# Optimization experiments

Measured on AMD Instinct MI355X. Metric: run time of the kernel, lower is better.

## Reference

```python
import jax, jax.numpy as jnp
import numpy as np

B, N, HID, H, FFN, E = 1, 50000, 96, 8, 384, 800000
D = HID // H
SCALE = float(np.sqrt(D))


def _layernorm(x, g, b, eps=1e-5):
    mu = jnp.mean(x, axis=-1, keepdims=True)
    var = jnp.var(x, axis=-1, keepdims=True)
    return (x - mu) * jax.lax.rsqrt(var + eps) * g + b


def setup_inputs() -> dict:
    key = jax.random.key(0)
    ks = jax.random.split(key, 20)
    std = 0.02
    inp = {
        "x": jax.random.normal(ks[0], (B, N, HID), dtype=jnp.float32),
        "edge_index": jax.random.randint(ks[1], (2, E), 0, B * N, dtype=jnp.int32),
        "ln1_g": jnp.ones((HID,), jnp.float32),
        "ln1_b": jnp.zeros((HID,), jnp.float32),
        "Wq": jax.random.normal(ks[2], (HID, HID), jnp.float32) * std,
        "bq": jnp.zeros((HID,), jnp.float32),
        "Wk": jax.random.normal(ks[3], (HID, HID), jnp.float32) * std,
        "bk": jnp.zeros((HID,), jnp.float32),
        "Wv": jax.random.normal(ks[4], (HID, HID), jnp.float32) * std,
        "bv": jnp.zeros((HID,), jnp.float32),
        "Wo": jax.random.normal(ks[5], (HID, HID), jnp.float32) * std,
        "bo": jnp.zeros((HID,), jnp.float32),
        "ln2_g": jnp.ones((HID,), jnp.float32),
        "ln2_b": jnp.zeros((HID,), jnp.float32),
        "W1": jax.random.normal(ks[6], (HID, FFN), jnp.float32) * std,
        "b1": jnp.zeros((FFN,), jnp.float32),
        "W2": jax.random.normal(ks[7], (FFN, HID), jnp.float32) * std,
        "b2": jnp.zeros((HID,), jnp.float32),
    }
    return inp


def _sparse_attn(q, k, v, edge_index):
    # q,k,v: [B*N, H, D]; edge_index: [2, E]
    src_idx = edge_index[0].astype(jnp.int32)
    dst_idx = edge_index[1].astype(jnp.int32)
    src = k[src_idx]                                # [E, H, D]
    dest = q[dst_idx]                               # [E, H, D]
    score = jnp.sum(src * dest, axis=-1, keepdims=True) / SCALE  # [E, H, 1]
    score = jnp.exp(jnp.clip(score, -5.0, 5.0))
    msg = v[src_idx] * score                        # [E, H, D]
    wV = jax.ops.segment_sum(msg, dst_idx, num_segments=B * N)   # [B*N, H, D]
    Z = jax.ops.segment_sum(score, dst_idx, num_segments=B * N)  # [B*N, H, 1]
    return wV / (Z + 1e-6)


def reference(x, edge_index, ln1_g, ln1_b, Wq, bq, Wk, bk, Wv, bv, Wo, bo,
              ln2_g, ln2_b, W1, b1, W2, b2):
    # --- self-attention block ---
    y = _layernorm(x, ln1_g, ln1_b)                 # [B, N, HID]
    q = (y @ Wq + bq).reshape(B * N, H, D)
    k = (y @ Wk + bk).reshape(B * N, H, D)
    v = (y @ Wv + bv).reshape(B * N, H, D)
    a = _sparse_attn(q, k, v, edge_index)           # [B*N, H, D]
    a = a.reshape(B, N, HID)
    y = a @ Wo + bo
    x = x + y
    # --- FFN block ---
    y = _layernorm(x, ln2_g, ln2_b)
    y = jax.nn.gelu(y @ W1 + b1, approximate=False)
    y = y @ W2 + b2
    return x + y
```

## Files before the change

### kernel.cpp

```cpp
#include <hip/hip_runtime.h>
#include <hip/hip_bf16.h>
#include <math.h>

#define NN 50000
#define HIDD 96
#define NH 8
#define HD 12
#define FFND 384
#define NE 800000
#define NB 98
#define BSTRIDE 12288

#define INV_SCALE 0.28867513459481287f
#define LOG2E 1.4426950408889634f

typedef short short8 __attribute__((ext_vector_type(8)));
typedef float f32x4 __attribute__((ext_vector_type(4)));
typedef float f32x2 __attribute__((ext_vector_type(2)));

__device__ __forceinline__ float bf2f(unsigned short u) {
    union { unsigned int i; float f; } c;
    c.i = ((unsigned int)u) << 16;
    return c.f;
}

__global__ __launch_bounds__(256) void prep(
    int* __restrict__ gcursor,
    const float* __restrict__ Wq, const float* __restrict__ Wk,
    const float* __restrict__ Wv, const float* __restrict__ Wo,
    const float* __restrict__ W1, const float* __restrict__ W2,
    __hip_bfloat16* __restrict__ wbuf,
    const float* __restrict__ x, const float* __restrict__ g1,
    const float* __restrict__ b1, __hip_bfloat16* __restrict__ ybf) {
    int b = blockIdx.x;
    int t = threadIdx.x;
    if (b == 0) {
        if (t < 128) gcursor[t] = t * BSTRIDE;
        return;
    }
    if (b < 433) {
        int idx = b - 1;
        const float* W; __hip_bfloat16* D; int K, N; int i;
        if (idx < 144)      { W = W1; D = wbuf + 36864; K = 96;  N = 384; i = idx * 256 + t; }
        else if (idx < 288) { W = W2; D = wbuf + 73728; K = 384; N = 96;  i = (idx - 144) * 256 + t; }
        else {
            int slab = (idx - 288) / 36;
            W = (slab == 0) ? Wq : (slab == 1) ? Wk : (slab == 2) ? Wv : Wo;
            D = wbuf + slab * 9216; K = 96; N = 96;
            i = ((idx - 288) % 36) * 256 + t;
        }
        if (i < K * N) {
            int n = i / K, k = i % K;
            D[i] = __float2bfloat16(W[k * N + n]);
        }
    } else {
        int row = (b - 433) * 4 + (t >> 6);
        int lane = t & 63;
        if (row >= NN) return;
        const float* xr = x + (size_t)row * HIDD;
        float v0 = xr[lane];
        float v1 = (lane < 32) ? xr[64 + lane] : 0.0f;
        float s = v0 + v1, q = v0 * v0 + v1 * v1;
#pragma unroll
        for (int o = 32; o > 0; o >>= 1) {
            s += __shfl_xor(s, o);
            q += __shfl_xor(q, o);
        }
        float mean = s * (1.0f / 96.0f);
        float var = q * (1.0f / 96.0f) - mean * mean;
        float rs = rsqrtf(var + 1e-5f);
        __hip_bfloat16* yr = ybf + (size_t)row * HIDD;
        yr[lane] = __float2bfloat16((v0 - mean) * rs * g1[lane] + b1[lane]);
        if (lane < 32)
            yr[64 + lane] = __float2bfloat16((v1 - mean) * rs * g1[64 + lane] + b1[64 + lane]);
    }
}

template<int K, int EPI, int SMODE>
__device__ __forceinline__ void gemm_body(
    const __hip_bfloat16* __restrict__ A, const __hip_bfloat16* __restrict__ BT,
    const float* __restrict__ bias, const __hip_bfloat16* __restrict__ R,
    void* __restrict__ Cptr, int ldc, int col0, int koff, int xb) {
    constexpr int BK = (K > 192) ? 192 : K;
    __shared__ __hip_bfloat16 Bs[96][BK + 8];
    int t = threadIdx.x;
    int lane = t & 63, wave = t >> 6;
    int row0 = xb * 128 + wave * 32;
    int lr = lane & 15, kg = lane >> 4;
    bool val0 = (row0 + 16 <= NN);
    bool val1 = (row0 + 32 <= NN);
    int ra0 = val0 ? row0 : 0;
    int ra1 = val1 ? (row0 + 16) : 0;
    const __hip_bfloat16* A0 = A + (size_t)(ra0 + lr) * K + kg * 8;
    const __hip_bfloat16* A1 = A + (size_t)(ra1 + lr) * K + kg * 8;
    f32x4 acc[2][6];
#pragma unroll
    for (int f = 0; f < 2; f++)
#pragma unroll
        for (int ct = 0; ct < 6; ct++) acc[f][ct] = (f32x4){0.f, 0.f, 0.f, 0.f};

    for (int k0 = 0; k0 < K; k0 += BK) {
        for (int i = t * 8; i < 96 * BK; i += 256 * 8) {
            int r = i / BK, c = i % BK;
            *(short8*)&Bs[r][c] = *(const short8*)&BT[(size_t)r * K + k0 + c];
        }
        __syncthreads();
#pragma unroll
        for (int kc = 0; kc < BK; kc += 32) {
            short8 a0 = *(const short8*)(A0 + k0 + kc);
            short8 a1 = *(const short8*)(A1 + k0 + kc);
#pragma unroll
            for (int ct = 0; ct < 6; ct++) {
                short8 bf_ = *(const short8*)&Bs[ct * 16 + lr][kc + kg * 8];
                acc[0][ct] = __builtin_amdgcn_mfma_f32_16x16x32_bf16(a0, bf_, acc[0][ct], 0, 0, 0);
                acc[1][ct] = __builtin_amdgcn_mfma_f32_16x16x32_bf16(a1, bf_, acc[1][ct], 0, 0, 0);
            }
        }
        __syncthreads();
    }

#pragma unroll
    for (int f = 0; f < 2; f++) {
        if (f == 0 ? !val0 : !val1) continue;
        int crow = row0 + f * 16 + kg * 4;
#pragma unroll
        for (int ct = 0; ct < 6; ct++) {
            int col = col0 + ct * 16 + lr;
            float bb = bias[col];
#pragma unroll
            for (int r = 0; r < 4; r++) {
                float o = acc[f][ct][r] + bb;
                if (EPI == 1)
                    o = 0.5f * o * (1.0f + erff(o * 0.70710678118654752f));
                if (EPI == 2)
                    o += __bfloat162float(R[(size_t)(crow + r) * 96 + col]);
                if (SMODE == 0)
                    ((float*)Cptr)[(size_t)(crow + r) * ldc + col] = o;
                else if (SMODE == 1)
                    ((__hip_bfloat16*)Cptr)[(size_t)(crow + r) * ldc + col] = __float2bfloat16(o);
                else {
                    unsigned int enc = (unsigned int)__builtin_amdgcn_cvt_pk_fp8_f32(o, o, 0, false);
                    ((unsigned char*)Cptr)[(size_t)(crow + r) * 192 + ((col - col0) / 12) * 24 + koff + ((col - col0) % 12)]
                        = (unsigned char)(enc & 0xffu);
                }
            }
        }
    }
}

__global__ __launch_bounds__(256) void scatter_qkv(
    const int* __restrict__ ei, int* __restrict__ gcursor,
    unsigned int* __restrict__ ebuf,
    const __hip_bfloat16* __restrict__ A, const __hip_bfloat16* __restrict__ wbuf,
    const float* __restrict__ bq, const float* __restrict__ bk,
    const float* __restrict__ bv,
    __hip_bfloat16* __restrict__ qbf, unsigned char* __restrict__ kv) {
    int b = blockIdx.x;
    if (b < 391) {
        __shared__ int lcount[128];
        __shared__ int lbase[128];
        int t = threadIdx.x;
        int e0 = b * 2048;
        if (t < 128) lcount[t] = 0;
        __syncthreads();
        int rank[8], dsts[8], srcv[8];
#pragma unroll
        for (int i = 0; i < 8; i++) {
            int e = e0 + t + i * 256;
            if (e < NE) {
                srcv[i] = ei[e];
                int d = ei[NE + e];
                dsts[i] = d;
                rank[i] = atomicAdd(&lcount[d >> 9], 1);
            } else dsts[i] = -1;
        }
        __syncthreads();
        if (t < 128) lbase[t] = lcount[t] ? atomicAdd(&gcursor[t], lcount[t]) : 0;
        __syncthreads();
#pragma unroll
        for (int i = 0; i < 8; i++) {
            if (dsts[i] >= 0) {
                int bk_ = dsts[i] >> 9;
                ebuf[lbase[bk_] + rank[i]] =
                    ((unsigned int)dsts[i] << 16) | (unsigned int)srcv[i];
            }
        }
    } else {
        int idx = b - 391;
        int y = idx / 391, xb = idx % 391;
        if (y == 0)
            gemm_body<96, 0, 1>(A, wbuf, bq, nullptr, qbf, 96, 0, 0, xb);
        else if (y == 1)
            gemm_body<96, 0, 2>(A, wbuf + 9216, bk, nullptr, kv, 0, 0, 0, xb);
        else
            gemm_body<96, 0, 2>(A, wbuf + 18432, bv, nullptr, kv, 0, 0, 12, xb);
    }
}

__global__ __launch_bounds__(1024) void bucket_build(
    const unsigned int* __restrict__ ebuf, const int* __restrict__ gcursor,
    uint2* __restrict__ rowrange, unsigned short* __restrict__ srcs) {
    __shared__ int cnt[512];
    int b = blockIdx.x;
    int t = threadIdx.x;
    int n0 = b * 512;
    int beg = b * BSTRIDE;
    int end = gcursor[b];
    if (t < 512) cnt[t] = 0;
    __syncthreads();
    for (int e = beg + t; e < end; e += 1024)
        atomicAdd(&cnt[(ebuf[e] >> 16) - n0], 1);
    __syncthreads();
    int my = (t < 512) ? cnt[t] : 0;
    for (int off = 1; off < 512; off <<= 1) {
        int v = (t >= off && t < 512) ? cnt[t - off] : 0;
        __syncthreads();
        if (t < 512) cnt[t] += v;
        __syncthreads();
    }
    int excl = (t > 0 && t < 512) ? cnt[t - 1] : 0;
    int base = beg + excl;
    if (t < 512 && n0 + t < NN)
        rowrange[n0 + t] = make_uint2((unsigned)base, (unsigned)(base + my));
    __syncthreads();
    if (t < 512) cnt[t] = base;
    __syncthreads();
    for (int e = beg + t; e < end; e += 1024) {
        unsigned int u = ebuf[e];
        int pos = atomicAdd(&cnt[(u >> 16) - n0], 1);
        srcs[pos] = (unsigned short)(u & 0xffffu);
    }
}

__global__ __launch_bounds__(256) void proj_ln(
    const __hip_bfloat16* __restrict__ A, const __hip_bfloat16* __restrict__ BT,
    const float* __restrict__ bias, const float* __restrict__ R,
    const float* __restrict__ g2, const float* __restrict__ b2v,
    __hip_bfloat16* __restrict__ x2, __hip_bfloat16* __restrict__ ybf) {
    constexpr int K = 96;
    __shared__ __hip_bfloat16 Bs[96][K + 8];
    int t = threadIdx.x;
    int lane = t & 63, wave = t >> 6;
    int row0 = blockIdx.x * 128 + wave * 32;
    int lr = lane & 15, kg = lane >> 4;
    bool val0 = (row0 + 16 <= NN);
    bool val1 = (row0 + 32 <= NN);
    int ra0 = val0 ? row0 : 0;
    int ra1 = val1 ? (row0 + 16) : 0;
    const __hip_bfloat16* A0 = A + (size_t)(ra0 + lr) * K + kg * 8;
    const __hip_bfloat16* A1 = A + (size_t)(ra1 + lr) * K + kg * 8;
    f32x4 acc[2][6];
#pragma unroll
    for (int f = 0; f < 2; f++)
#pragma unroll
        for (int ct = 0; ct < 6; ct++) acc[f][ct] = (f32x4){0.f, 0.f, 0.f, 0.f};

    for (int i = t * 8; i < 96 * K; i += 256 * 8) {
        int r = i / K, c = i % K;
        *(short8*)&Bs[r][c] = *(const short8*)&BT[(size_t)r * K + c];
    }
    __syncthreads();
#pragma unroll
    for (int kc = 0; kc < K; kc += 32) {
        short8 a0 = *(const short8*)(A0 + kc);
        short8 a1 = *(const short8*)(A1 + kc);
#pragma unroll
        for (int ct = 0; ct < 6; ct++) {
            short8 bf_ = *(const short8*)&Bs[ct * 16 + lr][kc + kg * 8];
            acc[0][ct] = __builtin_amdgcn_mfma_f32_16x16x32_bf16(a0, bf_, acc[0][ct], 0, 0, 0);
            acc[1][ct] = __builtin_amdgcn_mfma_f32_16x16x32_bf16(a1, bf_, acc[1][ct], 0, 0, 0);
        }
    }

    float bo_[6], gv[6], bv_[6];
#pragma unroll
    for (int ct = 0; ct < 6; ct++) {
        int col = ct * 16 + lr;
        bo_[ct] = bias[col];
        gv[ct]  = g2[col];
        bv_[ct] = b2v[col];
    }
#pragma unroll
    for (int f = 0; f < 2; f++) {
        if (f == 0 ? !val0 : !val1) continue;
        int crow = row0 + f * 16 + kg * 4;
#pragma unroll
        for (int r = 0; r < 4; r++) {
            int row = crow + r;
            float o[6], s1 = 0.f, s2 = 0.f;
#pragma unroll
            for (int ct = 0; ct < 6; ct++) {
                int col = ct * 16 + lr;
                float val = acc[f][ct][r] + bo_[ct] + R[(size_t)row * 96 + col];
                o[ct] = val; s1 += val; s2 += val * val;
            }
#pragma unroll
            for (int m = 1; m < 16; m <<= 1) {
                s1 += __shfl_xor(s1, m);
                s2 += __shfl_xor(s2, m);
            }
            float mu = s1 * (1.0f / 96.0f);
            float var = s2 * (1.0f / 96.0f) - mu * mu;
            float rs = rsqrtf(var + 1e-5f);
#pragma unroll
            for (int ct = 0; ct < 6; ct++) {
                int col = ct * 16 + lr;
                x2[(size_t)row * 96 + col] = __float2bfloat16(o[ct]);
                ybf[(size_t)row * 96 + col] =
                    __float2bfloat16((o[ct] - mu) * rs * gv[ct] + bv_[ct]);
            }
        }
    }
}

__global__ __launch_bounds__(256) void ffn_fused(
    const __hip_bfloat16* __restrict__ ybf, const __hip_bfloat16* __restrict__ W1T,
    const __hip_bfloat16* __restrict__ W2T, const float* __restrict__ b1,
    const float* __restrict__ b2v, const __hip_bfloat16* __restrict__ x2,
    float* __restrict__ out) {
    __shared__ __hip_bfloat16 hlds[64][392];
    __shared__ __hip_bfloat16 Bs[96][104];
    int t = threadIdx.x, lane = t & 63, wave = t >> 6;
    int row0 = blockIdx.x * 64;
    int lr = lane & 15, kg = lane >> 4;
    int rw = row0 + wave * 16;
    bool valid = (rw + 16 <= NN);
    int ra = valid ? rw : 0;

    short8 af[3];
#pragma unroll
    for (int kc = 0; kc < 3; kc++)
        af[kc] = *(const short8*)&ybf[(size_t)(ra + lr) * 96 + kc * 32 + kg * 8];

    for (int s = 0; s < 4; s++) {
        for (int i = t * 8; i < 96 * 96; i += 256 * 8) {
            int r = i / 96, c = i % 96;
            *(short8*)&Bs[r][c] = *(const short8*)&W1T[(size_t)(s * 96 + r) * 96 + c];
        }
        __syncthreads();
        f32x4 acc[6];
#pragma unroll
        for (int ct = 0; ct < 6; ct++) acc[ct] = (f32x4){0.f, 0.f, 0.f, 0.f};
#pragma unroll
        for (int kc = 0; kc < 3; kc++) {
#pragma unroll
            for (int ct = 0; ct < 6; ct++) {
                short8 bf_ = *(const short8*)&Bs[ct * 16 + lr][kc * 32 + kg * 8];
                acc[ct] = __builtin_amdgcn_mfma_f32_16x16x32_bf16(af[kc], bf_, acc[ct], 0, 0, 0);
            }
        }
#pragma unroll
        for (int ct = 0; ct < 6; ct++) {
            int col = s * 96 + ct * 16 + lr;
            float bb = b1[col];
#pragma unroll
            for (int r = 0; r < 4; r++) {
                float o = acc[ct][r] + bb;
                o = 0.5f * o * (1.0f + erff(o * 0.70710678118654752f));
                hlds[wave * 16 + kg * 4 + r][col] = __float2bfloat16(o);
            }
        }
        __syncthreads();
    }

    f32x4 acc2[6];
#pragma unroll
    for (int ct = 0; ct < 6; ct++) acc2[ct] = (f32x4){0.f, 0.f, 0.f, 0.f};
    for (int c = 0; c < 4; c++) {
        for (int i = t * 8; i < 96 * 96; i += 256 * 8) {
            int r = i / 96, cc = i % 96;
            *(short8*)&Bs[r][cc] = *(const short8*)&W2T[(size_t)r * 384 + c * 96 + cc];
        }
        __syncthreads();
#pragma unroll
        for (int kc = 0; kc < 3; kc++) {
            short8 a = *(const short8*)&hlds[wave * 16 + lr][c * 96 + kc * 32 + kg * 8];
#pragma unroll
            for (int ct = 0; ct < 6; ct++) {
                short8 bf_ = *(const short8*)&Bs[ct * 16 + lr][kc * 32 + kg * 8];
                acc2[ct] = __builtin_amdgcn_mfma_f32_16x16x32_bf16(a, bf_, acc2[ct], 0, 0, 0);
            }
        }
        __syncthreads();
    }

    if (valid) {
        int crow = rw + kg * 4;
#pragma unroll
        for (int ct = 0; ct < 6; ct++) {
            int col = ct * 16 + lr;
            float bb = b2v[col];
#pragma unroll
            for (int r = 0; r < 4; r++) {
                float o = acc2[ct][r] + bb
                        + __bfloat162float(x2[(size_t)(crow + r) * 96 + col]);
                out[(size_t)(crow + r) * 96 + col] = o;
            }
        }
    }
}

__global__ __launch_bounds__(256) void attn_gather(
    const __hip_bfloat16* __restrict__ qbf, const unsigned char* __restrict__ kv,
    const uint2* __restrict__ rowrange, const unsigned short* __restrict__ srcs,
    __hip_bfloat16* __restrict__ abf) {
    int wave = (blockIdx.x * blockDim.x + threadIdx.x) >> 6;
    int lane = threadIdx.x & 63;
    if (wave >= NN) return;
    int dst = wave;
    int h = lane & 7;
    int eslot = lane >> 3;
    float qf[12];
    {
        const uint2* qp = (const uint2*)(qbf + (size_t)dst * HIDD + h * HD);
        uint2 u0 = qp[0], u1 = qp[1], u2 = qp[2];
        unsigned int w[6] = {u0.x, u0.y, u1.x, u1.y, u2.x, u2.y};
#pragma unroll
        for (int i = 0; i < 6; i++) {
            qf[2 * i]     = bf2f((unsigned short)(w[i] & 0xffffu));
            qf[2 * i + 1] = bf2f((unsigned short)(w[i] >> 16));
        }
    }
    uint2 rr = rowrange[dst];
    int beg = (int)rr.x, end = (int)rr.y;
    float acc[12];
#pragma unroll
    for (int i = 0; i < 12; i++) acc[i] = 0.0f;
    float zz = 0.0f;

    int e = beg + eslot;
    bool has = e < end;
    uint2 cA, cB, cC;
    if (has) {
        int src = (int)srcs[e];
        const uint2* kp = (const uint2*)(kv + (size_t)src * 192 + h * 24);
        cA = kp[0]; cB = kp[1]; cC = kp[2];
    }
    while (has) {
        int en = e + 8;
        bool hasn = en < end;
        uint2 nA, nB, nC;
        if (hasn) {
            int srcn = (int)srcs[en];
            const uint2* kp = (const uint2*)(kv + (size_t)srcn * 192 + h * 24);
            nA = kp[0]; nB = kp[1]; nC = kp[2];
        }
        f32x2 p;
        float dot = 0.0f;
        p = __builtin_amdgcn_cvt_pk_f32_fp8(cA.x, false); dot += p[0] * qf[0]  + p[1] * qf[1];
        p = __builtin_amdgcn_cvt_pk_f32_fp8(cA.x, true);  dot += p[0] * qf[2]  + p[1] * qf[3];
        p = __builtin_amdgcn_cvt_pk_f32_fp8(cA.y, false); dot += p[0] * qf[4]  + p[1] * qf[5];
        p = __builtin_amdgcn_cvt_pk_f32_fp8(cA.y, true);  dot += p[0] * qf[6]  + p[1] * qf[7];
        p = __builtin_amdgcn_cvt_pk_f32_fp8(cB.x, false); dot += p[0] * qf[8]  + p[1] * qf[9];
        p = __builtin_amdgcn_cvt_pk_f32_fp8(cB.x, true);  dot += p[0] * qf[10] + p[1] * qf[11];
        float s = fminf(fmaxf(dot * INV_SCALE, -5.0f), 5.0f);
        float sc = exp2f(s * LOG2E);
        p = __builtin_amdgcn_cvt_pk_f32_fp8(cB.y, false); acc[0]  += p[0] * sc; acc[1]  += p[1] * sc;
        p = __builtin_amdgcn_cvt_pk_f32_fp8(cB.y, true);  acc[2]  += p[0] * sc; acc[3]  += p[1] * sc;
        p = __builtin_amdgcn_cvt_pk_f32_fp8(cC.x, false); acc[4]  += p[0] * sc; acc[5]  += p[1] * sc;
        p = __builtin_amdgcn_cvt_pk_f32_fp8(cC.x, true);  acc[6]  += p[0] * sc; acc[7]  += p[1] * sc;
        p = __builtin_amdgcn_cvt_pk_f32_fp8(cC.y, false); acc[8]  += p[0] * sc; acc[9]  += p[1] * sc;
        p = __builtin_amdgcn_cvt_pk_f32_fp8(cC.y, true);  acc[10] += p[0] * sc; acc[11] += p[1] * sc;
        zz += sc;
        cA = nA; cB = nB; cC = nC;
        e = en; has = hasn;
    }
#pragma unroll
    for (int m = 8; m < 64; m <<= 1) {
#pragma unroll
        for (int i = 0; i < 12; i++) acc[i] += __shfl_xor(acc[i], m);
        zz += __shfl_xor(zz, m);
    }
    if (eslot == 0) {
        float inv = 1.0f / (zz + 1e-6f);
        __hip_bfloat16* ar = abf + (size_t)dst * HIDD + h * HD;
#pragma unroll
        for (int i = 0; i < 12; i++) ar[i] = __float2bfloat16(acc[i] * inv);
    }
}

extern "C" void kernel_launch(void* const* d_in, const int* in_sizes, int n_in,
                              void* d_out, int out_size, void* d_ws, size_t ws_size,
                              hipStream_t stream) {
    const float* x     = (const float*)d_in[0];
    const int*   ei    = (const int*)d_in[1];
    const float* ln1_g = (const float*)d_in[2];
    const float* ln1_b = (const float*)d_in[3];
    const float* Wq    = (const float*)d_in[4];
    const float* bq    = (const float*)d_in[5];
    const float* Wk    = (const float*)d_in[6];
    const float* bk    = (const float*)d_in[7];
    const float* Wv    = (const float*)d_in[8];
    const float* bv    = (const float*)d_in[9];
    const float* Wo    = (const float*)d_in[10];
    const float* bo    = (const float*)d_in[11];
    const float* ln2_g = (const float*)d_in[12];
    const float* ln2_b = (const float*)d_in[13];
    const float* W1    = (const float*)d_in[14];
    const float* b1    = (const float*)d_in[15];
    const float* W2    = (const float*)d_in[16];
    const float* b2    = (const float*)d_in[17];
    float* out = (float*)d_out;

    float* ws = (float*)d_ws;
    const size_t NF = (size_t)NN * HIDD;
    __hip_bfloat16* qbf = (__hip_bfloat16*)ws;
    unsigned char*  kv  = (unsigned char*)(ws + NF / 2);
    __hip_bfloat16* abf = (__hip_bfloat16*)(ws + NF / 2 + NF);
    __hip_bfloat16* x2  = (__hip_bfloat16*)(ws + 2 * NF);
    __hip_bfloat16* ybf = (__hip_bfloat16*)(ws + 2 * NF + NF / 2);
    int* ibase = (int*)(ws + 3 * NF);
    uint2* rowrange = (uint2*)ibase;
    unsigned short* srcs = (unsigned short*)(ibase + 2 * NN);
    int* gcursor = ibase + 2 * NN + (NB * BSTRIDE + 1) / 2;
    unsigned int* ebuf = (unsigned int*)(gcursor + 128);
    __hip_bfloat16* wbuf = (__hip_bfloat16*)(ws + 3 * NF + NF / 2);
    __hip_bfloat16* WoT = wbuf + 27648;
    __hip_bfloat16* W1T = wbuf + 36864;
    __hip_bfloat16* W2T = wbuf + 73728;

    const int MT = (NN + 127) / 128;
    const int FT = (NN + 63) / 64;

    prep<<<433 + 12500, 256, 0, stream>>>(gcursor, Wq, Wk, Wv, Wo, W1, W2, wbuf,
                                          x, ln1_g, ln1_b, ybf);
    scatter_qkv<<<391 + 3 * MT, 256, 0, stream>>>(ei, gcursor, ebuf,
                                                  ybf, wbuf, bq, bk, bv, qbf, kv);
    bucket_build<<<NB, 1024, 0, stream>>>(ebuf, gcursor, rowrange, srcs);
    attn_gather<<<(NN + 3) / 4, 256, 0, stream>>>(qbf, kv, rowrange, srcs, abf);
    proj_ln<<<MT, 256, 0, stream>>>(abf, WoT, bo, x, ln2_g, ln2_b, x2, ybf);
    ffn_fused<<<FT, 256, 0, stream>>>(ybf, W1T, W2T, b1, b2, x2, out);
}
```

Baseline: 143.1 us.

## Split fused FFN into two persistent kernels with LDS-resident weight slabs

Replaces the single fused FFN kernel with two persistent kernels. ffn1_p keeps one 96-column slab of W1 in LDS per block and writes GELU output to a global bf16 hidden buffer. ffn2_p keeps a 48-column slab of W2 in LDS, reads the hidden buffer back and adds the residual. The goal is to stop reloading the weights per 64-row tile, cut the barriers, and give each wave two 16-row fragments for more MFMA reuse. The cost is a round trip of about 38 MB of hidden activations through global memory, stored in workspace that reuses the dead q/kv/attention buffers.

```diff
diff --git a/kernel.cpp b/kernel.cpp
--- a/kernel.cpp
+++ b/kernel.cpp
@@ -313,88 +313,122 @@
     }
 }
 
-__global__ __launch_bounds__(256) void ffn_fused(
+__global__ __launch_bounds__(256) void ffn1_p(
     const __hip_bfloat16* __restrict__ ybf, const __hip_bfloat16* __restrict__ W1T,
-    const __hip_bfloat16* __restrict__ W2T, const float* __restrict__ b1,
+    const float* __restrict__ b1, __hip_bfloat16* __restrict__ hbf) {
+    __shared__ __hip_bfloat16 Bs[96][104];
+    int t = threadIdx.x, lane = t & 63, wave = t >> 6;
+    int s = blockIdx.y;
+    int lr = lane & 15, kg = lane >> 4;
+    const __hip_bfloat16* slab = W1T + (size_t)s * 96 * 96;
+    for (int i = t * 8; i < 96 * 96; i += 256 * 8) {
+        int r = i / 96, c = i % 96;
+        *(short8*)&Bs[r][c] = *(const short8*)&slab[r * 96 + c];
+    }
+    __syncthreads();
+    float bb[6];
+#pragma unroll
+    for (int ct = 0; ct < 6; ct++) bb[ct] = b1[s * 96 + ct * 16 + lr];
+
+    for (int tile = blockIdx.x; tile < 391; tile += 98) {
+        int row0 = tile * 128 + wave * 32;
+        bool val0 = (row0 + 16 <= NN);
+        bool val1 = (row0 + 32 <= NN);
+        int ra0 = val0 ? row0 : 0;
+        int ra1 = val1 ? (row0 + 16) : 0;
+        short8 a0[3], a1[3];
+#pragma unroll
+        for (int kc = 0; kc < 3; kc++) {
+            a0[kc] = *(const short8*)&ybf[(size_t)(ra0 + lr) * 96 + kc * 32 + kg * 8];
+            a1[kc] = *(const short8*)&ybf[(size_t)(ra1 + lr) * 96 + kc * 32 + kg * 8];
+        }
+        f32x4 acc[2][6];
+#pragma unroll
+        for (int f = 0; f < 2; f++)
+#pragma unroll
+            for (int ct = 0; ct < 6; ct++) acc[f][ct] = (f32x4){0.f, 0.f, 0.f, 0.f};
+#pragma unroll
+        for (int kc = 0; kc < 3; kc++) {
+#pragma unroll
+            for (int ct = 0; ct < 6; ct++) {
+                short8 bf_ = *(const short8*)&Bs[ct * 16 + lr][kc * 32 + kg * 8];
+                acc[0][ct] = __builtin_amdgcn_mfma_f32_16x16x32_bf16(a0[kc], bf_, acc[0][ct], 0, 0, 0);
+                acc[1][ct] = __builtin_amdgcn_mfma_f32_16x16x32_bf16(a1[kc], bf_, acc[1][ct], 0, 0, 0);
+            }
+        }
+#pragma unroll
+        for (int f = 0; f < 2; f++) {
+            if (f == 0 ? !val0 : !val1) continue;
+            int crow = row0 + f * 16 + kg * 4;
+#pragma unroll
+            for (int ct = 0; ct < 6; ct++) {
+                int col = s * 96 + ct * 16 + lr;
+#pragma unroll
+                for (int r = 0; r < 4; r++) {
+                    float o = acc[f][ct][r] + bb[ct];
+                    o = 0.5f * o * (1.0f + erff(o * 0.70710678118654752f));
+                    hbf[(size_t)(crow + r) * FFND + col] = __float2bfloat16(o);
+                }
+            }
+        }
+    }
+}
+
+__global__ __launch_bounds__(256) void ffn2_p(
+    const __hip_bfloat16* __restrict__ hbf, const __hip_bfloat16* __restrict__ W2T,
     const float* __restrict__ b2v, const __hip_bfloat16* __restrict__ x2,
     float* __restrict__ out) {
-    __shared__ __hip_bfloat16 hlds[64][392];
-    __shared__ __hip_bfloat16 Bs[96][104];
+    __shared__ __hip_bfloat16 Bs[4][48][104];
     int t = threadIdx.x, lane = t & 63, wave = t >> 6;
-    int row0 = blockIdx.x * 64;
+    int ch = blockIdx.y;
     int lr = lane & 15, kg = lane >> 4;
-    int rw = row0 + wave * 16;
-    bool valid = (rw + 16 <= NN);
-    int ra = valid ? rw : 0;
-
-    short8 af[3];
-#pragma unroll
-    for (int kc = 0; kc < 3; kc++)
-        af[kc] = *(const short8*)&ybf[(size_t)(ra + lr) * 96 + kc * 32 + kg * 8];
-
-    for (int s = 0; s < 4; s++) {
-        for (int i = t * 8; i < 96 * 96; i += 256 * 8) {
-            int r = i / 96, c = i % 96;
-            *(short8*)&Bs[r][c] = *(const short8*)&W1T[(size_t)(s * 96 + r) * 96 + c];
-        }
-        __syncthreads();
-        f32x4 acc[6];
-#pragma unroll
-        for (int ct = 0; ct < 6; ct++) acc[ct] = (f32x4){0.f, 0.f, 0.f, 0.f};
-#pragma unroll
-        for (int kc = 0; kc < 3; kc++) {
-#pragma unroll
-            for (int ct = 0; ct < 6; ct++) {
-                short8 bf_ = *(const short8*)&Bs[ct * 16 + lr][kc * 32 + kg * 8];
-                acc[ct] = __builtin_amdgcn_mfma_f32_16x16x32_bf16(af[kc], bf_, acc[ct], 0, 0, 0);
-            }
-        }
-#pragma unroll
-        for (int ct = 0; ct < 6; ct++) {
-            int col = s * 96 + ct * 16 + lr;
-            float bb = b1[col];
-#pragma unroll
-            for (int r = 0; r < 4; r++) {
-                float o = acc[ct][r] + bb;
-                o = 0.5f * o * (1.0f + erff(o * 0.70710678118654752f));
-                hlds[wave * 16 + kg * 4 + r][col] = __float2bfloat16(o);
-            }
-        }
-        __syncthreads();
-    }
-
-    f32x4 acc2[6];
-#pragma unroll
-    for (int ct = 0; ct < 6; ct++) acc2[ct] = (f32x4){0.f, 0.f, 0.f, 0.f};
-    for (int c = 0; c < 4; c++) {
-        for (int i = t * 8; i < 96 * 96; i += 256 * 8) {
-            int r = i / 96, cc = i % 96;
-            *(short8*)&Bs[r][cc] = *(const short8*)&W2T[(size_t)r * 384 + c * 96 + cc];
-        }
-        __syncthreads();
-#pragma unroll
-        for (int kc = 0; kc < 3; kc++) {
-            short8 a = *(const short8*)&hlds[wave * 16 + lr][c * 96 + kc * 32 + kg * 8];
-#pragma unroll
-            for (int ct = 0; ct < 6; ct++) {
-                short8 bf_ = *(const short8*)&Bs[ct * 16 + lr][kc * 32 + kg * 8];
-                acc2[ct] = __builtin_amdgcn_mfma_f32_16x16x32_bf16(a, bf_, acc2[ct], 0, 0, 0);
-            }
-        }
-        __syncthreads();
-    }
-
-    if (valid) {
-        int crow = rw + kg * 4;
-#pragma unroll
-        for (int ct = 0; ct < 6; ct++) {
-            int col = ct * 16 + lr;
-            float bb = b2v[col];
-#pragma unroll
-            for (int r = 0; r < 4; r++) {
-                float o = acc2[ct][r] + bb
-                        + __bfloat162float(x2[(size_t)(crow + r) * 96 + col]);
-                out[(size_t)(crow + r) * 96 + col] = o;
+    const __hip_bfloat16* wslab = W2T + (size_t)ch * 48 * 384;
+    for (int i = t * 8; i < 48 * 384; i += 256 * 8) {
+        int r = i / 384, c = i % 384;
+        *(short8*)&Bs[c / 96][r][c % 96] = *(const short8*)&wslab[(size_t)r * 384 + c];
+    }
+    __syncthreads();
+    float bb[3];
+#pragma unroll
+    for (int ct = 0; ct < 3; ct++) bb[ct] = b2v[ch * 48 + ct * 16 + lr];
+
+    for (int tile = blockIdx.x; tile < 391; tile += 196) {
+        int row0 = tile * 128 + wave * 32;
+        bool val0 = (row0 + 16 <= NN);
+        bool val1 = (row0 + 32 <= NN);
+        int ra0 = val0 ? row0 : 0;
+        int ra1 = val1 ? (row0 + 16) : 0;
+        const __hip_bfloat16* H0 = hbf + (size_t)(ra0 + lr) * FFND + kg * 8;
+        const __hip_bfloat16* H1 = hbf + (size_t)(ra1 + lr) * FFND + kg * 8;
+        f32x4 acc[2][3];
+#pragma unroll
+        for (int f = 0; f < 2; f++)
+#pragma unroll
+            for (int ct = 0; ct < 3; ct++) acc[f][ct] = (f32x4){0.f, 0.f, 0.f, 0.f};
+#pragma unroll
+        for (int kc = 0; kc < 12; kc++) {
+            short8 a0 = *(const short8*)(H0 + kc * 32);
+            short8 a1 = *(const short8*)(H1 + kc * 32);
+#pragma unroll
+            for (int ct = 0; ct < 3; ct++) {
+                short8 bf_ = *(const short8*)&Bs[kc / 3][ct * 16 + lr][(kc % 3) * 32 + kg * 8];
+                acc[0][ct] = __builtin_amdgcn_mfma_f32_16x16x32_bf16(a0, bf_, acc[0][ct], 0, 0, 0);
+                acc[1][ct] = __builtin_amdgcn_mfma_f32_16x16x32_bf16(a1, bf_, acc[1][ct], 0, 0, 0);
+            }
+        }
+#pragma unroll
+        for (int f = 0; f < 2; f++) {
+            if (f == 0 ? !val0 : !val1) continue;
+            int crow = row0 + f * 16 + kg * 4;
+#pragma unroll
+            for (int ct = 0; ct < 3; ct++) {
+                int col = ch * 48 + ct * 16 + lr;
+#pragma unroll
+                for (int r = 0; r < 4; r++) {
+                    float o = acc[f][ct][r] + bb[ct]
+                            + __bfloat162float(x2[(size_t)(crow + r) * 96 + col]);
+                    out[(size_t)(crow + r) * 96 + col] = o;
+                }
             }
         }
     }
@@ -507,6 +541,7 @@
     __hip_bfloat16* qbf = (__hip_bfloat16*)ws;
     unsigned char*  kv  = (unsigned char*)(ws + NF / 2);
     __hip_bfloat16* abf = (__hip_bfloat16*)(ws + NF / 2 + NF);
+    __hip_bfloat16* hbf = (__hip_bfloat16*)ws;
     __hip_bfloat16* x2  = (__hip_bfloat16*)(ws + 2 * NF);
     __hip_bfloat16* ybf = (__hip_bfloat16*)(ws + 2 * NF + NF / 2);
     int* ibase = (int*)(ws + 3 * NF);
@@ -520,7 +555,6 @@
     __hip_bfloat16* W2T = wbuf + 73728;
 
     const int MT = (NN + 127) / 128;
-    const int FT = (NN + 63) / 64;
 
     prep<<<433 + 12500, 256, 0, stream>>>(gcursor, Wq, Wk, Wv, Wo, W1, W2, wbuf,
                                           x, ln1_g, ln1_b, ybf);
@@ -529,5 +563,12 @@
     bucket_build<<<NB, 1024, 0, stream>>>(ebuf, gcursor, rowrange, srcs);
     attn_gather<<<(NN + 3) / 4, 256, 0, stream>>>(qbf, kv, rowrange, srcs, abf);
     proj_ln<<<MT, 256, 0, stream>>>(abf, WoT, bo, x, ln2_g, ln2_b, x2, ybf);
-    ffn_fused<<<FT, 256, 0, stream>>>(ybf, W1T, W2T, b1, b2, x2, out);
-}
+    {
+        dim3 g(98, 4);
+        ffn1_p<<<g, 256, 0, stream>>>(ybf, W1T, b1, hbf);
+    }
+    {
+        dim3 g(196, 2);
+        ffn2_p<<<g, 256, 0, stream>>>(hbf, W2T, b2, x2, out);
+    }
+}
```

New measurement: 139.3 us. 1.03x faster.

## Merge QKV GEMM blocks and split fused FFN into two kernels

Applied to the files above, without the earlier changes.

The QKV projection now runs one block per 128-row tile that loads A fragments once and loops over the three weight slabs, replacing three separate blocks that each reloaded A. The fused FFN kernel, which kept the 384-wide hidden activations in a large LDS buffer, is split into ffn1_p, which writes the GELU output to a bf16 global buffer reusing workspace, and ffn2_p, which reads it back and does the second GEMM in two column chunks. The split is meant to cut LDS use and raise occupancy. In exchange it adds a roughly 38 MB global round trip and one more kernel launch.

```diff
diff --git a/kernel.cpp b/kernel.cpp
--- a/kernel.cpp
+++ b/kernel.cpp
@@ -76,78 +76,6 @@
     }
 }
 
-template<int K, int EPI, int SMODE>
-__device__ __forceinline__ void gemm_body(
-    const __hip_bfloat16* __restrict__ A, const __hip_bfloat16* __restrict__ BT,
-    const float* __restrict__ bias, const __hip_bfloat16* __restrict__ R,
-    void* __restrict__ Cptr, int ldc, int col0, int koff, int xb) {
-    constexpr int BK = (K > 192) ? 192 : K;
-    __shared__ __hip_bfloat16 Bs[96][BK + 8];
-    int t = threadIdx.x;
-    int lane = t & 63, wave = t >> 6;
-    int row0 = xb * 128 + wave * 32;
-    int lr = lane & 15, kg = lane >> 4;
-    bool val0 = (row0 + 16 <= NN);
-    bool val1 = (row0 + 32 <= NN);
-    int ra0 = val0 ? row0 : 0;
-    int ra1 = val1 ? (row0 + 16) : 0;
-    const __hip_bfloat16* A0 = A + (size_t)(ra0 + lr) * K + kg * 8;
-    const __hip_bfloat16* A1 = A + (size_t)(ra1 + lr) * K + kg * 8;
-    f32x4 acc[2][6];
-#pragma unroll
-    for (int f = 0; f < 2; f++)
-#pragma unroll
-        for (int ct = 0; ct < 6; ct++) acc[f][ct] = (f32x4){0.f, 0.f, 0.f, 0.f};
-
-    for (int k0 = 0; k0 < K; k0 += BK) {
-        for (int i = t * 8; i < 96 * BK; i += 256 * 8) {
-            int r = i / BK, c = i % BK;
-            *(short8*)&Bs[r][c] = *(const short8*)&BT[(size_t)r * K + k0 + c];
-        }
-        __syncthreads();
-#pragma unroll
-        for (int kc = 0; kc < BK; kc += 32) {
-            short8 a0 = *(const short8*)(A0 + k0 + kc);
-            short8 a1 = *(const short8*)(A1 + k0 + kc);
-#pragma unroll
-            for (int ct = 0; ct < 6; ct++) {
-                short8 bf_ = *(const short8*)&Bs[ct * 16 + lr][kc + kg * 8];
-                acc[0][ct] = __builtin_amdgcn_mfma_f32_16x16x32_bf16(a0, bf_, acc[0][ct], 0, 0, 0);
-                acc[1][ct] = __builtin_amdgcn_mfma_f32_16x16x32_bf16(a1, bf_, acc[1][ct], 0, 0, 0);
-            }
-        }
-        __syncthreads();
-    }
-
-#pragma unroll
-    for (int f = 0; f < 2; f++) {
-        if (f == 0 ? !val0 : !val1) continue;
-        int crow = row0 + f * 16 + kg * 4;
-#pragma unroll
-        for (int ct = 0; ct < 6; ct++) {
-            int col = col0 + ct * 16 + lr;
-            float bb = bias[col];
-#pragma unroll
-            for (int r = 0; r < 4; r++) {
-                float o = acc[f][ct][r] + bb;
-                if (EPI == 1)
-                    o = 0.5f * o * (1.0f + erff(o * 0.70710678118654752f));
-                if (EPI == 2)
-                    o += __bfloat162float(R[(size_t)(crow + r) * 96 + col]);
-                if (SMODE == 0)
-                    ((float*)Cptr)[(size_t)(crow + r) * ldc + col] = o;
-                else if (SMODE == 1)
-                    ((__hip_bfloat16*)Cptr)[(size_t)(crow + r) * ldc + col] = __float2bfloat16(o);
-                else {
-                    unsigned int enc = (unsigned int)__builtin_amdgcn_cvt_pk_fp8_f32(o, o, 0, false);
-                    ((unsigned char*)Cptr)[(size_t)(crow + r) * 192 + ((col - col0) / 12) * 24 + koff + ((col - col0) % 12)]
-                        = (unsigned char)(enc & 0xffu);
-                }
-            }
-        }
-    }
-}
-
 __global__ __launch_bounds__(256) void scatter_qkv(
     const int* __restrict__ ei, int* __restrict__ gcursor,
     unsigned int* __restrict__ ebuf,
@@ -156,10 +84,10 @@
     const float* __restrict__ bv,
     __hip_bfloat16* __restrict__ qbf, unsigned char* __restrict__ kv) {
     int b = blockIdx.x;
+    int t = threadIdx.x;
     if (b < 391) {
         __shared__ int lcount[128];
         __shared__ int lbase[128];
-        int t = threadIdx.x;
         int e0 = b * 2048;
         if (t < 128) lcount[t] = 0;
         __syncthreads();
@@ -186,14 +114,68 @@
             }
         }
     } else {
-        int idx = b - 391;
-        int y = idx / 391, xb = idx % 391;
-        if (y == 0)
-            gemm_body<96, 0, 1>(A, wbuf, bq, nullptr, qbf, 96, 0, 0, xb);
-        else if (y == 1)
-            gemm_body<96, 0, 2>(A, wbuf + 9216, bk, nullptr, kv, 0, 0, 0, xb);
-        else
-            gemm_body<96, 0, 2>(A, wbuf + 18432, bv, nullptr, kv, 0, 0, 12, xb);
+        __shared__ __hip_bfloat16 Bs[96][104];
+        int xb = b - 391;
+        int lane = t & 63, wave = t >> 6;
+        int row0 = xb * 128 + wave * 32;
+        int lr = lane & 15, kg = lane >> 4;
+        bool val0 = (row0 + 16 <= NN);
+        bool val1 = (row0 + 32 <= NN);
+        int ra0 = val0 ? row0 : 0;
+        int ra1 = val1 ? (row0 + 16) : 0;
+        short8 a0[3], a1[3];
+#pragma unroll
+        for (int kc = 0; kc < 3; kc++) {
+            a0[kc] = *(const short8*)&A[(size_t)(ra0 + lr) * 96 + kc * 32 + kg * 8];
+            a1[kc] = *(const short8*)&A[(size_t)(ra1 + lr) * 96 + kc * 32 + kg * 8];
+        }
+        for (int y = 0; y < 3; y++) {
+            const __hip_bfloat16* slab = wbuf + y * 9216;
+            for (int i = t * 8; i < 96 * 96; i += 256 * 8) {
+                int r = i / 96, c = i % 96;
+                *(short8*)&Bs[r][c] = *(const short8*)&slab[r * 96 + c];
+            }
+            __syncthreads();
+            f32x4 acc[2][6];
+#pragma unroll
+            for (int f = 0; f < 2; f++)
+#pragma unroll
+                for (int ct = 0; ct < 6; ct++) acc[f][ct] = (f32x4){0.f, 0.f, 0.f, 0.f};
+#pragma unroll
+            for (int kc = 0; kc < 3; kc++) {
+#pragma unroll
+                for (int ct = 0; ct < 6; ct++) {
+                    short8 bf_ = *(const short8*)&Bs[ct * 16 + lr][kc * 32 + kg * 8];
+                    acc[0][ct] = __builtin_amdgcn_mfma_f32_16x16x32_bf16(a0[kc], bf_, acc[0][ct], 0, 0, 0);
+                    acc[1][ct] = __builtin_amdgcn_mfma_f32_16x16x32_bf16(a1[kc], bf_, acc[1][ct], 0, 0, 0);
+                }
+            }
+            const float* bias = (y == 0) ? bq : (y == 1) ? bk : bv;
+            int koff = (y == 2) ? 12 : 0;
+#pragma unroll
+            for (int f = 0; f < 2; f++) {
+                if (f == 0 ? !val0 : !val1) continue;
+                int crow = row0 + f * 16 + kg * 4;
+#pragma unroll
+                for (int ct = 0; ct < 6; ct++) {
+                    int col = ct * 16 + lr;
+                    float bb = bias[col];
+#pragma unroll
+                    for (int r = 0; r < 4; r++) {
+                        float o = acc[f][ct][r] + bb;
+                        if (y == 0) {
+                            qbf[(size_t)(crow + r) * HIDD + col] = __float2bfloat16(o);
+                        } else {
+                            unsigned int enc =
+                                (unsigned int)__builtin_amdgcn_cvt_pk_fp8_f32(o, o, 0, false);
+                            kv[(size_t)(crow + r) * 192 + (col / 12) * 24 + koff + (col % 12)]
+                                = (unsigned char)(enc & 0xffu);
+                        }
+                    }
+                }
+            }
+            __syncthreads();
+        }
     }
 }
 
@@ -313,29 +295,25 @@
     }
 }
 
-__global__ __launch_bounds__(256) void ffn_fused(
+__global__ __launch_bounds__(256) void ffn1_p(
     const __hip_bfloat16* __restrict__ ybf, const __hip_bfloat16* __restrict__ W1T,
-    const __hip_bfloat16* __restrict__ W2T, const float* __restrict__ b1,
-    const float* __restrict__ b2v, const __hip_bfloat16* __restrict__ x2,
-    float* __restrict__ out) {
-    __shared__ __hip_bfloat16 hlds[64][392];
+    const float* __restrict__ b1, __hip_bfloat16* __restrict__ hbf) {
     __shared__ __hip_bfloat16 Bs[96][104];
     int t = threadIdx.x, lane = t & 63, wave = t >> 6;
-    int row0 = blockIdx.x * 64;
     int lr = lane & 15, kg = lane >> 4;
-    int rw = row0 + wave * 16;
-    bool valid = (rw + 16 <= NN);
-    int ra = valid ? rw : 0;
-
+    int row0 = blockIdx.x * 64 + wave * 16;
+    bool valid = (row0 + 16 <= NN);
+    int ra = valid ? row0 : 0;
     short8 af[3];
 #pragma unroll
     for (int kc = 0; kc < 3; kc++)
         af[kc] = *(const short8*)&ybf[(size_t)(ra + lr) * 96 + kc * 32 + kg * 8];
 
     for (int s = 0; s < 4; s++) {
+        const __hip_bfloat16* slab = W1T + (size_t)s * 96 * 96;
         for (int i = t * 8; i < 96 * 96; i += 256 * 8) {
             int r = i / 96, c = i % 96;
-            *(short8*)&Bs[r][c] = *(const short8*)&W1T[(size_t)(s * 96 + r) * 96 + c];
+            *(short8*)&Bs[r][c] = *(const short8*)&slab[r * 96 + c];
         }
         __syncthreads();
         f32x4 acc[6];
@@ -349,54 +327,72 @@
                 acc[ct] = __builtin_amdgcn_mfma_f32_16x16x32_bf16(af[kc], bf_, acc[ct], 0, 0, 0);
             }
         }
-#pragma unroll
-        for (int ct = 0; ct < 6; ct++) {
-            int col = s * 96 + ct * 16 + lr;
-            float bb = b1[col];
-#pragma unroll
-            for (int r = 0; r < 4; r++) {
-                float o = acc[ct][r] + bb;
-                o = 0.5f * o * (1.0f + erff(o * 0.70710678118654752f));
-                hlds[wave * 16 + kg * 4 + r][col] = __float2bfloat16(o);
-            }
-        }
-        __syncthreads();
-    }
-
-    f32x4 acc2[6];
-#pragma unroll
-    for (int ct = 0; ct < 6; ct++) acc2[ct] = (f32x4){0.f, 0.f, 0.f, 0.f};
-    for (int c = 0; c < 4; c++) {
-        for (int i = t * 8; i < 96 * 96; i += 256 * 8) {
-            int r = i / 96, cc = i % 96;
-            *(short8*)&Bs[r][cc] = *(const short8*)&W2T[(size_t)r * 384 + c * 96 + cc];
-        }
-        __syncthreads();
-#pragma unroll
-        for (int kc = 0; kc < 3; kc++) {
-            short8 a = *(const short8*)&hlds[wave * 16 + lr][c * 96 + kc * 32 + kg * 8];
+        if (valid) {
+            int crow = row0 + kg * 4;
 #pragma unroll
             for (int ct = 0; ct < 6; ct++) {
-                short8 bf_ = *(const short8*)&Bs[ct * 16 + lr][kc * 32 + kg * 8];
-                acc2[ct] = __builtin_amdgcn_mfma_f32_16x16x32_bf16(a, bf_, acc2[ct], 0, 0, 0);
-            }
-        }
-        __syncthreads();
-    }
-
-    if (valid) {
-        int crow = rw + kg * 4;
-#pragma unroll
-        for (int ct = 0; ct < 6; ct++) {
-            int col = ct * 16 + lr;
-            float bb = b2v[col];
-#pragma unroll
-            for (int r = 0; r < 4; r++) {
-                float o = acc2[ct][r] + bb
-                        + __bfloat162float(x2[(size_t)(crow + r) * 96 + col]);
-                out[(size_t)(crow + r) * 96 + col] = o;
-            }
-        }
+                int col = s * 96 + ct * 16 + lr;
+                float bb = b1[col];
+#pragma unroll
+                for (int r = 0; r < 4; r++) {
+                    float o = acc[ct][r] + bb;
+                    o = 0.5f * o * (1.0f + erff(o * 0.70710678118654752f));
+                    hbf[(size_t)(crow + r) * FFND + col] = __float2bfloat16(o);
+                }
+            }
+        }
+        __syncthreads();
+    }
+}
+
+__global__ __launch_bounds__(256) void ffn2_p(
+    const __hip_bfloat16* __restrict__ hbf, const __hip_bfloat16* __restrict__ W2T,
+    const float* __restrict__ b2v, const __hip_bfloat16* __restrict__ x2,
+    float* __restrict__ out) {
+    __shared__ __hip_bfloat16 Bs[4][48][104];
+    int t = threadIdx.x, lane = t & 63, wave = t >> 6;
+    int lr = lane & 15, kg = lane >> 4;
+    int row0 = blockIdx.x * 64 + wave * 16;
+    bool valid = (row0 + 16 <= NN);
+    int ra = valid ? row0 : 0;
+    short8 hf[12];
+#pragma unroll
+    for (int kc = 0; kc < 12; kc++)
+        hf[kc] = *(const short8*)&hbf[(size_t)(ra + lr) * FFND + kc * 32 + kg * 8];
+
+    for (int ch = 0; ch < 2; ch++) {
+        const __hip_bfloat16* wslab = W2T + (size_t)ch * 48 * 384;
+        for (int i = t * 8; i < 48 * 384; i += 256 * 8) {
+            int r = i / 384, c = i % 384;
+            *(short8*)&Bs[c / 96][r][c % 96] = *(const short8*)&wslab[(size_t)r * 384 + c];
+        }
+        __syncthreads();
+        f32x4 acc[3];
+#pragma unroll
+        for (int ct = 0; ct < 3; ct++) acc[ct] = (f32x4){0.f, 0.f, 0.f, 0.f};
+#pragma unroll
+        for (int kc = 0; kc < 12; kc++) {
+#pragma unroll
+            for (int ct = 0; ct < 3; ct++) {
+                short8 bf_ = *(const short8*)&Bs[kc / 3][ct * 16 + lr][(kc % 3) * 32 + kg * 8];
+                acc[ct] = __builtin_amdgcn_mfma_f32_16x16x32_bf16(hf[kc], bf_, acc[ct], 0, 0, 0);
+            }
+        }
+        if (valid) {
+            int crow = row0 + kg * 4;
+#pragma unroll
+            for (int ct = 0; ct < 3; ct++) {
+                int col = ch * 48 + ct * 16 + lr;
+                float bb = b2v[col];
+#pragma unroll
+                for (int r = 0; r < 4; r++) {
+                    float o = acc[ct][r] + bb
+                            + __bfloat162float(x2[(size_t)(crow + r) * 96 + col]);
+                    out[(size_t)(crow + r) * 96 + col] = o;
+                }
+            }
+        }
+        __syncthreads();
     }
 }
 
@@ -507,6 +503,7 @@
     __hip_bfloat16* qbf = (__hip_bfloat16*)ws;
     unsigned char*  kv  = (unsigned char*)(ws + NF / 2);
     __hip_bfloat16* abf = (__hip_bfloat16*)(ws + NF / 2 + NF);
+    __hip_bfloat16* hbf = (__hip_bfloat16*)ws;
     __hip_bfloat16* x2  = (__hip_bfloat16*)(ws + 2 * NF);
     __hip_bfloat16* ybf = (__hip_bfloat16*)(ws + 2 * NF + NF / 2);
     int* ibase = (int*)(ws + 3 * NF);
@@ -524,10 +521,11 @@
 
     prep<<<433 + 12500, 256, 0, stream>>>(gcursor, Wq, Wk, Wv, Wo, W1, W2, wbuf,
                                           x, ln1_g, ln1_b, ybf);
-    scatter_qkv<<<391 + 3 * MT, 256, 0, stream>>>(ei, gcursor, ebuf,
-                                                  ybf, wbuf, bq, bk, bv, qbf, kv);
+    scatter_qkv<<<391 + MT, 256, 0, stream>>>(ei, gcursor, ebuf,
+                                              ybf, wbuf, bq, bk, bv, qbf, kv);
     bucket_build<<<NB, 1024, 0, stream>>>(ebuf, gcursor, rowrange, srcs);
     attn_gather<<<(NN + 3) / 4, 256, 0, stream>>>(qbf, kv, rowrange, srcs, abf);
     proj_ln<<<MT, 256, 0, stream>>>(abf, WoT, bo, x, ln2_g, ln2_b, x2, ybf);
-    ffn_fused<<<FT, 256, 0, stream>>>(ybf, W1T, W2T, b1, b2, x2, out);
-}
+    ffn1_p<<<FT, 256, 0, stream>>>(ybf, W1T, b1, hbf);
+    ffn2_p<<<FT, 256, 0, stream>>>(hbf, W2T, b2, x2, out);
+}
```

Result: faster. 134.1 us (-6.3%).
